# Kernel optimization log

Measured on AMD Instinct MI355X. Metric: run time of the kernel, lower is better.

Reference implementation:

```python
import jax, jax.numpy as jnp
import numpy as np

# Qwen3-MoE style config
B, S, D = 2, 2048, 2048        # batch, seqlen, hidden_size
E, I, TOPK = 64, 768, 8        # num_experts, moe_intermediate_size, num_experts_per_tok
M = B * S                      # tokens
CAP = 2 * (M * TOPK) // E


def setup_inputs() -> dict:
    key = jax.random.key(0)
    k0, k1, k2, k3, k4 = jax.random.split(key, 5)
    return {
        "x": jax.random.normal(k0, (B, S, D), jnp.float32),
        "router_weight": jax.random.normal(k1, (D, E), jnp.float32) * 0.02,
        "gate_proj": jax.random.normal(k2, (E, D, I), jnp.float32) * 0.02,
        "up_proj": jax.random.normal(k3, (E, D, I), jnp.float32) * 0.02,
        "down_proj": jax.random.normal(k4, (E, I, D), jnp.float32) * 0.02,
    }


def _moe(x, router_weight, gate_proj, up_proj, down_proj):
    b, s, d = x.shape
    xf = x.reshape(-1, d)                                  # [M, d]
    m = xf.shape[0]

    # ---- TokenChoiceTopKRouter: softmax scores, top-k, renormalize ----
    logits = xf @ router_weight                            # [M, E]
    probs = jax.nn.softmax(logits.astype(jnp.float32), axis=-1)
    topw, topi = jax.lax.top_k(probs, TOPK)                # [M, k]
    topw = topw / topw.sum(axis=-1, keepdims=True)         # norm_topk_prob

    flat_e = topi.reshape(-1)                              # [M*k] expert id per assignment
    flat_w = topw.reshape(-1).astype(x.dtype)              # [M*k] routing weight per assignment

    # ---- permute: sort assignments by expert (stable) ----
    order = jnp.argsort(flat_e)                            # [M*k]
    se = flat_e[order]                                     # sorted expert ids
    tok = order // TOPK                                    # source token per sorted assignment
    counts = jax.ops.segment_sum(jnp.ones_like(flat_e), flat_e, num_segments=E)
    starts = jnp.cumsum(counts) - counts                   # exclusive prefix sum
    pos = jnp.arange(m * TOPK) - starts[se]                # slot within expert's buffer
    valid = pos < CAP
    posc = jnp.minimum(pos, CAP - 1)

    # ---- dispatch to padded per-expert buffers [E, CAP, d] ----
    xe = jnp.zeros((E, CAP, d), x.dtype).at[se, pos].set(xf[tok], mode='drop')

    # ---- grouped SwiGLU experts (batched GEMMs) ----
    h = jax.nn.silu(jnp.einsum('ecd,edi->eci', xe, gate_proj)) \
        * jnp.einsum('ecd,edi->eci', xe, up_proj)          # [E, CAP, I]
    ye = jnp.einsum('eci,eid->ecd', h, down_proj)          # [E, CAP, d]

    # ---- unpermute + weighted combine ----
    contrib = jnp.where(valid[:, None], ye[se, posc], 0.0) * flat_w[order][:, None]
    out = jnp.zeros((m, d), x.dtype).at[tok].add(contrib)  # sum over topk per token
    return out.reshape(b, s, d)


def reference(x, router_weight, gate_proj, up_proj, down_proj):
    return _moe(x, router_weight, gate_proj, up_proj, down_proj)
```

## Files before the change

### kernel.cpp

```cpp
#include <hip/hip_runtime.h>
#include <hip/hip_bf16.h>

typedef __attribute__((ext_vector_type(4))) float f32x4;
typedef __attribute__((ext_vector_type(8))) short bf16x8;
typedef unsigned int   u32;
typedef unsigned short u16;

#define D_DIM 2048
#define I_DIM 768
#define NE    64
#define CAP   1024
#define NTOK  4096

__device__ __forceinline__ u32 cvt2(float a, float b) {
  __hip_bfloat162 hh = __float22bfloat162_rn(float2{a, b});
  union { __hip_bfloat162 h; u32 u; } c; c.h = hh; return c.u;
}
__device__ __forceinline__ u16 f2b(float f) {
  __hip_bfloat16 b = __float2bfloat16(f);
  union { __hip_bfloat16 b; u16 u; } c; c.b = b; return c.u;
}
__device__ __forceinline__ void glp16(const void* g, void* l) {
  __builtin_amdgcn_global_load_lds(
      (const __attribute__((address_space(1))) u32*)g,
      (__attribute__((address_space(3))) u32*)l, 16, 0, 0);
}

__global__ __launch_bounds__(256) void k_cvt_x(const float* __restrict__ x,
                                               u16* __restrict__ xb) {
  const size_t i = ((size_t)blockIdx.x * 256 + threadIdx.x) * 8;
  float4 v0 = *(const float4*)(x + i);
  float4 v1 = *(const float4*)(x + i + 4);
  uint4 o;
  o.x = cvt2(v0.x, v0.y); o.y = cvt2(v0.z, v0.w);
  o.z = cvt2(v1.x, v1.y); o.w = cvt2(v1.z, v1.w);
  *(uint4*)(xb + i) = o;
}

__global__ __launch_bounds__(256) void k_router(
    const float* __restrict__ x, const float* __restrict__ rw,
    int* __restrict__ counts, int* __restrict__ slot_token,
    float* __restrict__ slot_w)
{
  const int lane = threadIdx.x & 63;
  const int tok  = blockIdx.x * 4 + (threadIdx.x >> 6);
  const float* xr = x + (size_t)tok * D_DIM;

  float acc = 0.f;
  for (int d0 = 0; d0 < D_DIM; d0 += 64) {
    float xv = xr[d0 + lane];
    #pragma unroll
    for (int j = 0; j < 64; ++j) {
      float xj = __shfl(xv, j, 64);
      acc = fmaf(xj, rw[(size_t)(d0 + j) * NE + lane], acc);
    }
  }

  float v = acc; int vi = lane;
  float wk[8]; int ei[8];
  float mx0 = 0.f, wsum = 0.f;
  #pragma unroll
  for (int k = 0; k < 8; ++k) {
    float mv = v; int mi = vi;
    #pragma unroll
    for (int off = 32; off >= 1; off >>= 1) {
      float ov = __shfl_xor(mv, off, 64);
      int   oi = __shfl_xor(mi, off, 64);
      if (ov > mv || (ov == mv && oi < mi)) { mv = ov; mi = oi; }
    }
    if (k == 0) mx0 = mv;
    float ew = __expf(mv - mx0);
    wk[k] = ew; ei[k] = mi; wsum += ew;
    if (lane == mi) v = -3.4e38f;
  }

  if (lane == 0) {
    float inv = 1.f / wsum;
    #pragma unroll
    for (int k = 0; k < 8; ++k) {
      int ee   = ei[k];
      int slot = atomicAdd(&counts[ee], 1);
      if (slot < CAP) {
        slot_token[ee * CAP + slot] = tok;
        slot_w[ee * CAP + slot]     = wk[k] * inv;
      }
    }
  }
}

__global__ __launch_bounds__(256) void k_mlp1(
    const u16* __restrict__ xb, const float* __restrict__ gate,
    const float* __restrict__ up, const int* __restrict__ counts,
    const int* __restrict__ slot_token, u16* __restrict__ h)
{
  const int i   = blockIdx.x;
  const int xcd = i & 7;
  const int p   = i >> 3;
  const int mt  = p & 7;
  const int pe  = p >> 3;
  const int val = pe * 8 + xcd;
  const int e   = val / 12;
  const int nt  = val % 12;

  int cnt = counts[e]; if (cnt > CAP) cnt = CAP;
  const int m0 = mt * 128;
  if (m0 >= cnt) return;
  const int n0 = nt * 64;

  const int t = threadIdx.x;
  const int lane = t & 63, wv = t >> 6;
  const int li = lane & 15, gq = lane >> 4;
  const int wr = wv >> 1, wc = wv & 1;

  __shared__ u16 As[2][8 * 128 * 8];
  __shared__ u16 Bg[2][8 * 64 * 8];
  __shared__ u16 Bu[2][8 * 64 * 8];

  const int mh  = wv & 1;
  const int kgA = (wv >> 1) * 4;
  const int tok = slot_token[e * CAP + m0 + mh * 64 + lane];
  const u16* xrow = xb + (size_t)tok * D_DIM;

  const float* gb = gate + (size_t)e * D_DIM * I_DIM + n0 + lane;
  const float* ub = up   + (size_t)e * D_DIM * I_DIM + n0 + lane;

  f32x4 ag[4][2], au[4][2];
  #pragma unroll
  for (int m = 0; m < 4; ++m)
    #pragma unroll
    for (int n = 0; n < 2; ++n) {
      f32x4 z = {0.f, 0.f, 0.f, 0.f};
      ag[m][n] = z; au[m][n] = z;
    }

  float gv[2][8], uv[2][8];

  #pragma unroll
  for (int q = 0; q < 4; ++q) {
    const int kg = kgA + q;
    glp16(xrow + kg * 8, &As[0][(kg * 128 + mh * 64) * 8]);
  }
  #pragma unroll
  for (int c = 0; c < 2; ++c) {
    const int kg = wv * 2 + c;
    #pragma unroll
    for (int j = 0; j < 8; ++j) {
      gv[c][j] = gb[(size_t)(kg * 8 + j) * I_DIM];
      uv[c][j] = ub[(size_t)(kg * 8 + j) * I_DIM];
    }
  }

  int buf = 0;
  for (int kk = 0; kk < D_DIM; kk += 64) {
    #pragma unroll
    for (int c = 0; c < 2; ++c) {
      const int kg = wv * 2 + c;
      uint4 og, ou;
      og.x = cvt2(gv[c][0], gv[c][1]); og.y = cvt2(gv[c][2], gv[c][3]);
      og.z = cvt2(gv[c][4], gv[c][5]); og.w = cvt2(gv[c][6], gv[c][7]);
      ou.x = cvt2(uv[c][0], uv[c][1]); ou.y = cvt2(uv[c][2], uv[c][3]);
      ou.z = cvt2(uv[c][4], uv[c][5]); ou.w = cvt2(uv[c][6], uv[c][7]);
      *(uint4*)&Bg[buf][(kg * 64 + lane) * 8] = og;
      *(uint4*)&Bu[buf][(kg * 64 + lane) * 8] = ou;
    }
    __syncthreads();

    if (kk + 64 < D_DIM) {
      #pragma unroll
      for (int q = 0; q < 4; ++q) {
        const int kg = kgA + q;
        glp16(xrow + kk + 64 + kg * 8, &As[buf ^ 1][(kg * 128 + mh * 64) * 8]);
      }
      #pragma unroll
      for (int c = 0; c < 2; ++c) {
        const int kg = wv * 2 + c;
        #pragma unroll
        for (int j = 0; j < 8; ++j) {
          gv[c][j] = gb[(size_t)(kk + 64 + kg * 8 + j) * I_DIM];
          uv[c][j] = ub[(size_t)(kk + 64 + kg * 8 + j) * I_DIM];
        }
      }
    }

    #pragma unroll
    for (int kc = 0; kc < 2; ++kc) {
      const int kg = kc * 4 + gq;
      bf16x8 a0 = *(const bf16x8*)&As[buf][(kg * 128 + wr * 64 +      li) * 8];
      bf16x8 a1 = *(const bf16x8*)&As[buf][(kg * 128 + wr * 64 + 16 + li) * 8];
      bf16x8 a2 = *(const bf16x8*)&As[buf][(kg * 128 + wr * 64 + 32 + li) * 8];
      bf16x8 a3 = *(const bf16x8*)&As[buf][(kg * 128 + wr * 64 + 48 + li) * 8];
      bf16x8 g0 = *(const bf16x8*)&Bg[buf][(kg * 64 + wc * 32 +      li) * 8];
      bf16x8 g1 = *(const bf16x8*)&Bg[buf][(kg * 64 + wc * 32 + 16 + li) * 8];
      bf16x8 u0 = *(const bf16x8*)&Bu[buf][(kg * 64 + wc * 32 +      li) * 8];
      bf16x8 u1 = *(const bf16x8*)&Bu[buf][(kg * 64 + wc * 32 + 16 + li) * 8];
      ag[0][0] = __builtin_amdgcn_mfma_f32_16x16x32_bf16(a0, g0, ag[0][0], 0, 0, 0);
      ag[1][0] = __builtin_amdgcn_mfma_f32_16x16x32_bf16(a1, g0, ag[1][0], 0, 0, 0);
      ag[2][0] = __builtin_amdgcn_mfma_f32_16x16x32_bf16(a2, g0, ag[2][0], 0, 0, 0);
      ag[3][0] = __builtin_amdgcn_mfma_f32_16x16x32_bf16(a3, g0, ag[3][0], 0, 0, 0);
      ag[0][1] = __builtin_amdgcn_mfma_f32_16x16x32_bf16(a0, g1, ag[0][1], 0, 0, 0);
      ag[1][1] = __builtin_amdgcn_mfma_f32_16x16x32_bf16(a1, g1, ag[1][1], 0, 0, 0);
      ag[2][1] = __builtin_amdgcn_mfma_f32_16x16x32_bf16(a2, g1, ag[2][1], 0, 0, 0);
      ag[3][1] = __builtin_amdgcn_mfma_f32_16x16x32_bf16(a3, g1, ag[3][1], 0, 0, 0);
      au[0][0] = __builtin_amdgcn_mfma_f32_16x16x32_bf16(a0, u0, au[0][0], 0, 0, 0);
      au[1][0] = __builtin_amdgcn_mfma_f32_16x16x32_bf16(a1, u0, au[1][0], 0, 0, 0);
      au[2][0] = __builtin_amdgcn_mfma_f32_16x16x32_bf16(a2, u0, au[2][0], 0, 0, 0);
      au[3][0] = __builtin_amdgcn_mfma_f32_16x16x32_bf16(a3, u0, au[3][0], 0, 0, 0);
      au[0][1] = __builtin_amdgcn_mfma_f32_16x16x32_bf16(a0, u1, au[0][1], 0, 0, 0);
      au[1][1] = __builtin_amdgcn_mfma_f32_16x16x32_bf16(a1, u1, au[1][1], 0, 0, 0);
      au[2][1] = __builtin_amdgcn_mfma_f32_16x16x32_bf16(a2, u1, au[2][1], 0, 0, 0);
      au[3][1] = __builtin_amdgcn_mfma_f32_16x16x32_bf16(a3, u1, au[3][1], 0, 0, 0);
    }
    __syncthreads();
    buf ^= 1;
  }

  #pragma unroll
  for (int mf = 0; mf < 4; ++mf) {
    #pragma unroll
    for (int j = 0; j < 4; ++j) {
      const int slot = m0 + wr * 64 + mf * 16 + gq * 4 + j;
      u16* hr = h + (size_t)(e * CAP + slot) * I_DIM + n0 + wc * 32 + li;
      #pragma unroll
      for (int nf = 0; nf < 2; ++nf) {
        float gg = ag[mf][nf][j];
        float uu = au[mf][nf][j];
        hr[nf * 16] = f2b(gg * uu / (1.f + __expf(-gg)));
      }
    }
  }
}

__global__ __launch_bounds__(256) void k_mlp2(
    const u16* __restrict__ h, const float* __restrict__ down,
    const int* __restrict__ counts, const int* __restrict__ slot_token,
    const float* __restrict__ slot_w, float* __restrict__ out)
{
  const int i   = blockIdx.x;
  const int xcd = i & 7;
  const int p   = i >> 3;
  const int mt  = p & 7;
  const int pe  = p >> 3;
  const int val = pe * 8 + xcd;
  const int e   = val >> 4;
  const int nt  = val & 15;

  int cnt = counts[e]; if (cnt > CAP) cnt = CAP;
  const int m0 = mt * 128;
  if (m0 >= cnt) return;
  const int n0 = nt * 128;

  const int t = threadIdx.x;
  const int lane = t & 63, wv = t >> 6;
  const int li = lane & 15, gq = lane >> 4;
  const int wm = (wv >> 1) * 64, wn = (wv & 1) * 64;

  __shared__ u16 As[2][8 * 128 * 8];
  __shared__ u16 Bt[2][8 * 128 * 8];

  const int mh  = wv & 1;
  const int kgA = (wv >> 1) * 4;
  const u16* hrow = h + (size_t)(e * CAP + m0 + mh * 64 + lane) * I_DIM;

  const int nh  = wv >> 1;
  const int kgB = (wv & 1) * 4;
  const float* db = down + (size_t)e * I_DIM * D_DIM + n0 + nh * 64 + lane;

  f32x4 acc[4][4];
  #pragma unroll
  for (int m = 0; m < 4; ++m)
    #pragma unroll
    for (int n = 0; n < 4; ++n) { f32x4 z = {0.f,0.f,0.f,0.f}; acc[m][n] = z; }

  float dv[4][8];

  #pragma unroll
  for (int q = 0; q < 4; ++q) {
    const int kg = kgA + q;
    glp16(hrow + kg * 8, &As[0][(kg * 128 + mh * 64) * 8]);
  }
  #pragma unroll
  for (int c = 0; c < 4; ++c) {
    const int kg = kgB + c;
    #pragma unroll
    for (int j = 0; j < 8; ++j)
      dv[c][j] = db[(size_t)(kg * 8 + j) * D_DIM];
  }

  int buf = 0;
  for (int kk = 0; kk < I_DIM; kk += 64) {
    #pragma unroll
    for (int c = 0; c < 4; ++c) {
      const int kg = kgB + c;
      uint4 o;
      o.x = cvt2(dv[c][0], dv[c][1]); o.y = cvt2(dv[c][2], dv[c][3]);
      o.z = cvt2(dv[c][4], dv[c][5]); o.w = cvt2(dv[c][6], dv[c][7]);
      *(uint4*)&Bt[buf][(kg * 128 + nh * 64 + lane) * 8] = o;
    }
    __syncthreads();

    if (kk + 64 < I_DIM) {
      #pragma unroll
      for (int q = 0; q < 4; ++q) {
        const int kg = kgA + q;
        glp16(hrow + kk + 64 + kg * 8, &As[buf ^ 1][(kg * 128 + mh * 64) * 8]);
      }
      #pragma unroll
      for (int c = 0; c < 4; ++c) {
        const int kg = kgB + c;
        #pragma unroll
        for (int j = 0; j < 8; ++j)
          dv[c][j] = db[(size_t)(kk + 64 + kg * 8 + j) * D_DIM];
      }
    }

    #pragma unroll
    for (int kc = 0; kc < 2; ++kc) {
      const int kg = kc * 4 + gq;
      bf16x8 a[4], b[4];
      #pragma unroll
      for (int mf = 0; mf < 4; ++mf)
        a[mf] = *(const bf16x8*)&As[buf][(kg * 128 + wm + mf * 16 + li) * 8];
      #pragma unroll
      for (int nf = 0; nf < 4; ++nf)
        b[nf] = *(const bf16x8*)&Bt[buf][(kg * 128 + wn + nf * 16 + li) * 8];
      #pragma unroll
      for (int mf = 0; mf < 4; ++mf)
        #pragma unroll
        for (int nf = 0; nf < 4; ++nf)
          acc[mf][nf] = __builtin_amdgcn_mfma_f32_16x16x32_bf16(a[mf], b[nf], acc[mf][nf], 0, 0, 0);
    }
    __syncthreads();
    buf ^= 1;
  }

  #pragma unroll
  for (int mf = 0; mf < 4; ++mf) {
    #pragma unroll
    for (int j = 0; j < 4; ++j) {
      const int slot = m0 + wm + mf * 16 + gq * 4 + j;
      if (slot < cnt) {
        const int   tk  = slot_token[e * CAP + slot];
        const float wgt = slot_w[e * CAP + slot];
        float* orow = out + (size_t)tk * D_DIM + n0 + wn + li;
        #pragma unroll
        for (int nf = 0; nf < 4; ++nf)
          atomicAdd(&orow[nf * 16], wgt * acc[mf][nf][j]);
      }
    }
  }
}

extern "C" void kernel_launch(void* const* d_in, const int* in_sizes, int n_in,
                              void* d_out, int out_size, void* d_ws, size_t ws_size,
                              hipStream_t stream) {
  const float* x    = (const float*)d_in[0];
  const float* rw   = (const float*)d_in[1];
  const float* gate = (const float*)d_in[2];
  const float* up   = (const float*)d_in[3];
  const float* down = (const float*)d_in[4];
  float* out = (float*)d_out;

  char* ws = (char*)d_ws;
  int*   counts     = (int*)ws;
  int*   slot_token = (int*)(ws + 1024);
  float* slot_w     = (float*)(ws + 1024 + (size_t)NE * CAP * 4);
  u16*   xb         = (u16*)(ws + 1024 + (size_t)NE * CAP * 8);
  u16*   h          = (u16*)(ws + 1024 + (size_t)NE * CAP * 8
                                  + (size_t)NTOK * D_DIM * 2);

  hipMemsetAsync(counts, 0, NE * sizeof(int), stream);
  hipMemsetAsync(slot_token, 0, (size_t)NE * CAP * sizeof(int), stream);
  hipMemsetAsync(out, 0, (size_t)out_size * sizeof(float), stream);

  k_cvt_x <<<dim3((NTOK * D_DIM) / (256 * 8)), 256, 0, stream>>>(x, xb);
  k_router<<<dim3(NTOK / 4),                   256, 0, stream>>>(x, rw, counts, slot_token, slot_w);
  k_mlp1  <<<dim3(6144),                       256, 0, stream>>>(xb, gate, up, counts, slot_token, h);
  k_mlp2  <<<dim3(8192),                       256, 0, stream>>>(h, down, counts, slot_token, slot_w, out);
}
```

Measured before the change: 1.426 ms.

## Halve K-tile, restructure pipeline to one sync per step, raise occupancy

Both expert GEMM kernels now use a K step of 32 instead of 64, which halves the shared-memory buffers. The launch bounds request 4 blocks per CU. The loop is restructured into a prologue plus a steady state: it issues next-tile loads, runs the MFMAs on the current tile, then converts and stores the prefetched weights to the other buffer. This needs a single barrier per iteration instead of two. The aim is higher occupancy and better latency hiding. The trade-off is twice as many iterations with less MFMA work per barrier and possible register pressure from the occupancy hint.

```diff
diff --git a/kernel.cpp b/kernel.cpp
--- a/kernel.cpp
+++ b/kernel.cpp
@@ -88,7 +88,7 @@
   }
 }
 
-__global__ __launch_bounds__(256) void k_mlp1(
+__global__ __launch_bounds__(256, 4) void k_mlp1(
     const u16* __restrict__ xb, const float* __restrict__ gate,
     const float* __restrict__ up, const int* __restrict__ counts,
     const int* __restrict__ slot_token, u16* __restrict__ h)
@@ -112,12 +112,12 @@
   const int li = lane & 15, gq = lane >> 4;
   const int wr = wv >> 1, wc = wv & 1;
 
-  __shared__ u16 As[2][8 * 128 * 8];
-  __shared__ u16 Bg[2][8 * 64 * 8];
-  __shared__ u16 Bu[2][8 * 64 * 8];
+  __shared__ u16 As[2][4 * 128 * 8];
+  __shared__ u16 Bg[2][4 * 64 * 8];
+  __shared__ u16 Bu[2][4 * 64 * 8];
 
   const int mh  = wv & 1;
-  const int kgA = (wv >> 1) * 4;
+  const int kgA = (wv >> 1) * 2;
   const int tok = slot_token[e * CAP + m0 + mh * 64 + lane];
   const u16* xrow = xb + (size_t)tok * D_DIM;
 
@@ -133,66 +133,48 @@
       ag[m][n] = z; au[m][n] = z;
     }
 
-  float gv[2][8], uv[2][8];
-
-  #pragma unroll
-  for (int q = 0; q < 4; ++q) {
-    const int kg = kgA + q;
-    glp16(xrow + kg * 8, &As[0][(kg * 128 + mh * 64) * 8]);
-  }
-  #pragma unroll
-  for (int c = 0; c < 2; ++c) {
-    const int kg = wv * 2 + c;
-    #pragma unroll
-    for (int j = 0; j < 8; ++j) {
-      gv[c][j] = gb[(size_t)(kg * 8 + j) * I_DIM];
-      uv[c][j] = ub[(size_t)(kg * 8 + j) * I_DIM];
-    }
-  }
+  float gv[8], uv[8];
+
+  glp16(xrow + (kgA    ) * 8, &As[0][((kgA    ) * 128 + mh * 64) * 8]);
+  glp16(xrow + (kgA + 1) * 8, &As[0][((kgA + 1) * 128 + mh * 64) * 8]);
+  #pragma unroll
+  for (int j = 0; j < 8; ++j) {
+    gv[j] = gb[(size_t)(wv * 8 + j) * I_DIM];
+    uv[j] = ub[(size_t)(wv * 8 + j) * I_DIM];
+  }
+  {
+    uint4 og, ou;
+    og.x = cvt2(gv[0], gv[1]); og.y = cvt2(gv[2], gv[3]);
+    og.z = cvt2(gv[4], gv[5]); og.w = cvt2(gv[6], gv[7]);
+    ou.x = cvt2(uv[0], uv[1]); ou.y = cvt2(uv[2], uv[3]);
+    ou.z = cvt2(uv[4], uv[5]); ou.w = cvt2(uv[6], uv[7]);
+    *(uint4*)&Bg[0][(wv * 64 + lane) * 8] = og;
+    *(uint4*)&Bu[0][(wv * 64 + lane) * 8] = ou;
+  }
+  __syncthreads();
 
   int buf = 0;
-  for (int kk = 0; kk < D_DIM; kk += 64) {
-    #pragma unroll
-    for (int c = 0; c < 2; ++c) {
-      const int kg = wv * 2 + c;
-      uint4 og, ou;
-      og.x = cvt2(gv[c][0], gv[c][1]); og.y = cvt2(gv[c][2], gv[c][3]);
-      og.z = cvt2(gv[c][4], gv[c][5]); og.w = cvt2(gv[c][6], gv[c][7]);
-      ou.x = cvt2(uv[c][0], uv[c][1]); ou.y = cvt2(uv[c][2], uv[c][3]);
-      ou.z = cvt2(uv[c][4], uv[c][5]); ou.w = cvt2(uv[c][6], uv[c][7]);
-      *(uint4*)&Bg[buf][(kg * 64 + lane) * 8] = og;
-      *(uint4*)&Bu[buf][(kg * 64 + lane) * 8] = ou;
-    }
-    __syncthreads();
-
-    if (kk + 64 < D_DIM) {
-      #pragma unroll
-      for (int q = 0; q < 4; ++q) {
-        const int kg = kgA + q;
-        glp16(xrow + kk + 64 + kg * 8, &As[buf ^ 1][(kg * 128 + mh * 64) * 8]);
-      }
-      #pragma unroll
-      for (int c = 0; c < 2; ++c) {
-        const int kg = wv * 2 + c;
-        #pragma unroll
-        for (int j = 0; j < 8; ++j) {
-          gv[c][j] = gb[(size_t)(kk + 64 + kg * 8 + j) * I_DIM];
-          uv[c][j] = ub[(size_t)(kk + 64 + kg * 8 + j) * I_DIM];
-        }
-      }
-    }
-
-    #pragma unroll
-    for (int kc = 0; kc < 2; ++kc) {
-      const int kg = kc * 4 + gq;
-      bf16x8 a0 = *(const bf16x8*)&As[buf][(kg * 128 + wr * 64 +      li) * 8];
-      bf16x8 a1 = *(const bf16x8*)&As[buf][(kg * 128 + wr * 64 + 16 + li) * 8];
-      bf16x8 a2 = *(const bf16x8*)&As[buf][(kg * 128 + wr * 64 + 32 + li) * 8];
-      bf16x8 a3 = *(const bf16x8*)&As[buf][(kg * 128 + wr * 64 + 48 + li) * 8];
-      bf16x8 g0 = *(const bf16x8*)&Bg[buf][(kg * 64 + wc * 32 +      li) * 8];
-      bf16x8 g1 = *(const bf16x8*)&Bg[buf][(kg * 64 + wc * 32 + 16 + li) * 8];
-      bf16x8 u0 = *(const bf16x8*)&Bu[buf][(kg * 64 + wc * 32 +      li) * 8];
-      bf16x8 u1 = *(const bf16x8*)&Bu[buf][(kg * 64 + wc * 32 + 16 + li) * 8];
+  for (int kk = 0; kk < D_DIM; kk += 32) {
+    const bool more = (kk + 32) < D_DIM;
+    if (more) {
+      glp16(xrow + kk + 32 + (kgA    ) * 8, &As[buf ^ 1][((kgA    ) * 128 + mh * 64) * 8]);
+      glp16(xrow + kk + 32 + (kgA + 1) * 8, &As[buf ^ 1][((kgA + 1) * 128 + mh * 64) * 8]);
+      #pragma unroll
+      for (int j = 0; j < 8; ++j) {
+        gv[j] = gb[(size_t)(kk + 32 + wv * 8 + j) * I_DIM];
+        uv[j] = ub[(size_t)(kk + 32 + wv * 8 + j) * I_DIM];
+      }
+    }
+
+    {
+      bf16x8 a0 = *(const bf16x8*)&As[buf][(gq * 128 + wr * 64 +      li) * 8];
+      bf16x8 a1 = *(const bf16x8*)&As[buf][(gq * 128 + wr * 64 + 16 + li) * 8];
+      bf16x8 a2 = *(const bf16x8*)&As[buf][(gq * 128 + wr * 64 + 32 + li) * 8];
+      bf16x8 a3 = *(const bf16x8*)&As[buf][(gq * 128 + wr * 64 + 48 + li) * 8];
+      bf16x8 g0 = *(const bf16x8*)&Bg[buf][(gq * 64 + wc * 32 +      li) * 8];
+      bf16x8 g1 = *(const bf16x8*)&Bg[buf][(gq * 64 + wc * 32 + 16 + li) * 8];
+      bf16x8 u0 = *(const bf16x8*)&Bu[buf][(gq * 64 + wc * 32 +      li) * 8];
+      bf16x8 u1 = *(const bf16x8*)&Bu[buf][(gq * 64 + wc * 32 + 16 + li) * 8];
       ag[0][0] = __builtin_amdgcn_mfma_f32_16x16x32_bf16(a0, g0, ag[0][0], 0, 0, 0);
       ag[1][0] = __builtin_amdgcn_mfma_f32_16x16x32_bf16(a1, g0, ag[1][0], 0, 0, 0);
       ag[2][0] = __builtin_amdgcn_mfma_f32_16x16x32_bf16(a2, g0, ag[2][0], 0, 0, 0);
@@ -210,6 +192,16 @@
       au[2][1] = __builtin_amdgcn_mfma_f32_16x16x32_bf16(a2, u1, au[2][1], 0, 0, 0);
       au[3][1] = __builtin_amdgcn_mfma_f32_16x16x32_bf16(a3, u1, au[3][1], 0, 0, 0);
     }
+
+    if (more) {
+      uint4 og, ou;
+      og.x = cvt2(gv[0], gv[1]); og.y = cvt2(gv[2], gv[3]);
+      og.z = cvt2(gv[4], gv[5]); og.w = cvt2(gv[6], gv[7]);
+      ou.x = cvt2(uv[0], uv[1]); ou.y = cvt2(uv[2], uv[3]);
+      ou.z = cvt2(uv[4], uv[5]); ou.w = cvt2(uv[6], uv[7]);
+      *(uint4*)&Bg[buf ^ 1][(wv * 64 + lane) * 8] = og;
+      *(uint4*)&Bu[buf ^ 1][(wv * 64 + lane) * 8] = ou;
+    }
     __syncthreads();
     buf ^= 1;
   }
@@ -230,7 +222,7 @@
   }
 }
 
-__global__ __launch_bounds__(256) void k_mlp2(
+__global__ __launch_bounds__(256, 4) void k_mlp2(
     const u16* __restrict__ h, const float* __restrict__ down,
     const int* __restrict__ counts, const int* __restrict__ slot_token,
     const float* __restrict__ slot_w, float* __restrict__ out)
@@ -254,16 +246,16 @@
   const int li = lane & 15, gq = lane >> 4;
   const int wm = (wv >> 1) * 64, wn = (wv & 1) * 64;
 
-  __shared__ u16 As[2][8 * 128 * 8];
-  __shared__ u16 Bt[2][8 * 128 * 8];
+  __shared__ u16 As[2][4 * 128 * 8];
+  __shared__ u16 Bt[2][4 * 128 * 8];
 
   const int mh  = wv & 1;
-  const int kgA = (wv >> 1) * 4;
+  const int kgA = (wv >> 1) * 2;
   const u16* hrow = h + (size_t)(e * CAP + m0 + mh * 64 + lane) * I_DIM;
 
-  const int nh  = wv >> 1;
-  const int kgB = (wv & 1) * 4;
-  const float* db = down + (size_t)e * I_DIM * D_DIM + n0 + nh * 64 + lane;
+  const int nB  = t & 127;
+  const int kgB = (t >> 7) * 2;
+  const float* db = down + (size_t)e * I_DIM * D_DIM + n0 + nB;
 
   f32x4 acc[4][4];
   #pragma unroll
@@ -271,63 +263,60 @@
     #pragma unroll
     for (int n = 0; n < 4; ++n) { f32x4 z = {0.f,0.f,0.f,0.f}; acc[m][n] = z; }
 
-  float dv[4][8];
-
-  #pragma unroll
-  for (int q = 0; q < 4; ++q) {
-    const int kg = kgA + q;
-    glp16(hrow + kg * 8, &As[0][(kg * 128 + mh * 64) * 8]);
-  }
-  #pragma unroll
-  for (int c = 0; c < 4; ++c) {
-    const int kg = kgB + c;
+  float dv[2][8];
+
+  glp16(hrow + (kgA    ) * 8, &As[0][((kgA    ) * 128 + mh * 64) * 8]);
+  glp16(hrow + (kgA + 1) * 8, &As[0][((kgA + 1) * 128 + mh * 64) * 8]);
+  #pragma unroll
+  for (int c = 0; c < 2; ++c)
     #pragma unroll
     for (int j = 0; j < 8; ++j)
-      dv[c][j] = db[(size_t)(kg * 8 + j) * D_DIM];
-  }
+      dv[c][j] = db[(size_t)((kgB + c) * 8 + j) * D_DIM];
+  #pragma unroll
+  for (int c = 0; c < 2; ++c) {
+    uint4 o;
+    o.x = cvt2(dv[c][0], dv[c][1]); o.y = cvt2(dv[c][2], dv[c][3]);
+    o.z = cvt2(dv[c][4], dv[c][5]); o.w = cvt2(dv[c][6], dv[c][7]);
+    *(uint4*)&Bt[0][((kgB + c) * 128 + nB) * 8] = o;
+  }
+  __syncthreads();
 
   int buf = 0;
-  for (int kk = 0; kk < I_DIM; kk += 64) {
-    #pragma unroll
-    for (int c = 0; c < 4; ++c) {
-      const int kg = kgB + c;
-      uint4 o;
-      o.x = cvt2(dv[c][0], dv[c][1]); o.y = cvt2(dv[c][2], dv[c][3]);
-      o.z = cvt2(dv[c][4], dv[c][5]); o.w = cvt2(dv[c][6], dv[c][7]);
-      *(uint4*)&Bt[buf][(kg * 128 + nh * 64 + lane) * 8] = o;
-    }
-    __syncthreads();
-
-    if (kk + 64 < I_DIM) {
-      #pragma unroll
-      for (int q = 0; q < 4; ++q) {
-        const int kg = kgA + q;
-        glp16(hrow + kk + 64 + kg * 8, &As[buf ^ 1][(kg * 128 + mh * 64) * 8]);
-      }
-      #pragma unroll
-      for (int c = 0; c < 4; ++c) {
-        const int kg = kgB + c;
+  for (int kk = 0; kk < I_DIM; kk += 32) {
+    const bool more = (kk + 32) < I_DIM;
+    if (more) {
+      glp16(hrow + kk + 32 + (kgA    ) * 8, &As[buf ^ 1][((kgA    ) * 128 + mh * 64) * 8]);
+      glp16(hrow + kk + 32 + (kgA + 1) * 8, &As[buf ^ 1][((kgA + 1) * 128 + mh * 64) * 8]);
+      #pragma unroll
+      for (int c = 0; c < 2; ++c)
         #pragma unroll
         for (int j = 0; j < 8; ++j)
-          dv[c][j] = db[(size_t)(kk + 64 + kg * 8 + j) * D_DIM];
-      }
-    }
-
-    #pragma unroll
-    for (int kc = 0; kc < 2; ++kc) {
-      const int kg = kc * 4 + gq;
+          dv[c][j] = db[(size_t)(kk + 32 + (kgB + c) * 8 + j) * D_DIM];
+    }
+
+    {
       bf16x8 a[4], b[4];
       #pragma unroll
       for (int mf = 0; mf < 4; ++mf)
-        a[mf] = *(const bf16x8*)&As[buf][(kg * 128 + wm + mf * 16 + li) * 8];
+        a[mf] = *(const bf16x8*)&As[buf][(gq * 128 + wm + mf * 16 + li) * 8];
       #pragma unroll
       for (int nf = 0; nf < 4; ++nf)
-        b[nf] = *(const bf16x8*)&Bt[buf][(kg * 128 + wn + nf * 16 + li) * 8];
+        b[nf] = *(const bf16x8*)&Bt[buf][(gq * 128 + wn + nf * 16 + li) * 8];
       #pragma unroll
       for (int mf = 0; mf < 4; ++mf)
         #pragma unroll
         for (int nf = 0; nf < 4; ++nf)
           acc[mf][nf] = __builtin_amdgcn_mfma_f32_16x16x32_bf16(a[mf], b[nf], acc[mf][nf], 0, 0, 0);
+    }
+
+    if (more) {
+      #pragma unroll
+      for (int c = 0; c < 2; ++c) {
+        uint4 o;
+        o.x = cvt2(dv[c][0], dv[c][1]); o.y = cvt2(dv[c][2], dv[c][3]);
+        o.z = cvt2(dv[c][4], dv[c][5]); o.w = cvt2(dv[c][6], dv[c][7]);
+        *(uint4*)&Bt[buf ^ 1][((kgB + c) * 128 + nB) * 8] = o;
+      }
     }
     __syncthreads();
     buf ^= 1;
```

Result: faster. 1.373 ms (-3.7%).
